# Kernel optimization log

Measured on AMD Instinct MI355X. Metric: run time of the kernel, lower is better.

Reference implementation:

```python
import jax, jax.numpy as jnp
import numpy as np

D_MODEL = 1024
NUM_HEADS = 16
HEAD_DIM = D_MODEL // NUM_HEADS
SCALE = HEAD_DIM ** -0.5
BATCH = 4096
N_MODULES = 8


def setup_inputs() -> dict:
    key = jax.random.key(0)
    ks = jax.random.split(key, 7)
    s = 1.0 / np.sqrt(D_MODEL)
    return {
        "query": jax.random.normal(ks[0], (BATCH, D_MODEL), jnp.float32),
        "kv_stack": jax.random.normal(ks[1], (N_MODULES, BATCH, D_MODEL), jnp.float32),
        "Wq": jax.random.normal(ks[2], (D_MODEL, D_MODEL), jnp.float32) * s,
        "Wk": jax.random.normal(ks[3], (D_MODEL, D_MODEL), jnp.float32) * s,
        "Wv": jax.random.normal(ks[4], (D_MODEL, D_MODEL), jnp.float32) * s,
        "Wo": jax.random.normal(ks[5], (D_MODEL, D_MODEL), jnp.float32) * s,
        "bo": jnp.zeros((D_MODEL,), jnp.float32),
    }


def reference(query, kv_stack, Wq, Wk, Wv, Wo, bo):
    # query: [B, D]; kv_stack: [M, B, D] (stacked module representations)
    B = query.shape[0]
    M = kv_stack.shape[0]
    # projections (nn.Linear: x @ W.T), split into heads; seq_len == 1
    q = (query @ Wq.T).reshape(B, NUM_HEADS, HEAD_DIM)            # [B,H,hd]
    k = jnp.einsum("mbd,ed->mbe", kv_stack, Wk).reshape(M, B, NUM_HEADS, HEAD_DIM)
    v = jnp.einsum("mbd,ed->mbe", kv_stack, Wv).reshape(M, B, NUM_HEADS, HEAD_DIM)
    # scores over the single kv position: [M,B,H,1]
    scores = jnp.einsum("bhd,mbhd->mbh", q, k)[..., None] * SCALE
    attn_weights = jax.nn.softmax(scores, axis=-1)  # softmax over size-1 axis -> ones
    attn_output = attn_weights * v                   # [M,B,H,hd] (dropout is eval/no-op)
    attn_output = attn_output.reshape(M, B, D_MODEL)
    out = jnp.einsum("mbe,oe->mbo", attn_output, Wo) + bo + query  # residual per module
    return out  # [M, B, D] (stacked in kv order instead of the dict)
```

## Files before the change

### kernel.cpp

```cpp
#include <hip/hip_runtime.h>
#include <hip/hip_bf16.h>


typedef __attribute__((ext_vector_type(4))) float f32x4;
typedef __attribute__((ext_vector_type(8))) short short8;

#define D_MODEL 1024
#define BATCH   4096
#define M_ROWS  32768

__device__ __forceinline__ short f2bf(float f) {
    union { float f; unsigned u; } x; x.f = f;
    unsigned r = (x.u + 0x7fffu + ((x.u >> 16) & 1u)) >> 16;
    return (short)r;
}

__device__ __forceinline__ unsigned bfpk(float lo, float hi) {
    __hip_bfloat162 h = __float22bfloat162_rn(make_float2(lo, hi));
    unsigned u; __builtin_memcpy(&u, &h, 4); return u;
}

__device__ __forceinline__ short8 cvt8(float4 a, float4 b) {
    union { unsigned u[4]; short8 s; } r;
    r.u[0] = bfpk(a.x, a.y);
    r.u[1] = bfpk(a.z, a.w);
    r.u[2] = bfpk(b.x, b.y);
    r.u[3] = bfpk(b.z, b.w);
    return r.s;
}

__global__ __launch_bounds__(256) void cvt_kv_kernel(
        const float* __restrict__ in, short* __restrict__ outb) {
    const long n8 = (long)M_ROWS * D_MODEL / 8;
    long i = (long)blockIdx.x * 256 + threadIdx.x;
    const long stride = (long)gridDim.x * 256;
    for (; i < n8; i += stride) {
        const float4* p = (const float4*)(in + i * 8);
        float4 a = p[0], b = p[1];
        *reinterpret_cast<short8*>(outb + i * 8) = cvt8(a, b);
    }
}

__global__ __launch_bounds__(256) void fuse_w_kernel(
        const float* __restrict__ Wo, const float* __restrict__ Wv,
        short* __restrict__ Cw) {
    __shared__ __align__(16) short Ash[64][32];
    __shared__ __align__(16) short Bsh[64][32];
    const int t = threadIdx.x;
    const int lane = t & 63;
    const int w = t >> 6;
    const int wr = w >> 1, wc = w & 1;
    const int brow = blockIdx.y * 64;
    const int bcol = blockIdx.x * 64;

    f32x4 acc[2][2];
#pragma unroll
    for (int m = 0; m < 2; ++m)
#pragma unroll
        for (int n = 0; n < 2; ++n) acc[m][n] = (f32x4)(0.0f);

    for (int kt = 0; kt < 32; ++kt) {
        const float* ga = Wo + (size_t)(brow + (t >> 2)) * D_MODEL + kt * 32 + (t & 3) * 8;
        float4 a0 = *(const float4*)ga;
        float4 a1 = *(const float4*)(ga + 4);
        float4 bv[2];
#pragma unroll
        for (int j = 0; j < 2; ++j) {
            int lin = j * 256 + t;
            int e = lin >> 4, c4 = lin & 15;
            bv[j] = *(const float4*)(Wv + (size_t)(kt * 32 + e) * D_MODEL + bcol + c4 * 4);
        }
        *reinterpret_cast<short8*>(&Ash[t >> 2][(t & 3) * 8]) = cvt8(a0, a1);
#pragma unroll
        for (int j = 0; j < 2; ++j) {
            int lin = j * 256 + t;
            int e = lin >> 4, c4 = lin & 15;
            int d = c4 * 4;
            Bsh[d + 0][e] = f2bf(bv[j].x);
            Bsh[d + 1][e] = f2bf(bv[j].y);
            Bsh[d + 2][e] = f2bf(bv[j].z);
            Bsh[d + 3][e] = f2bf(bv[j].w);
        }
        __syncthreads();
        {
            const int r = lane & 15, q = lane >> 4;
            short8 af[2], bfr[2];
#pragma unroll
            for (int m = 0; m < 2; ++m)
                af[m] = *reinterpret_cast<const short8*>(&Ash[wr * 32 + m * 16 + r][q * 8]);
#pragma unroll
            for (int n = 0; n < 2; ++n)
                bfr[n] = *reinterpret_cast<const short8*>(&Bsh[wc * 32 + n * 16 + r][q * 8]);
#pragma unroll
            for (int m = 0; m < 2; ++m)
#pragma unroll
                for (int n = 0; n < 2; ++n)
                    acc[m][n] = __builtin_amdgcn_mfma_f32_16x16x32_bf16(
                        af[m], bfr[n], acc[m][n], 0, 0, 0);
        }
        __syncthreads();
    }

    const int r = lane & 15, q = lane >> 4;
#pragma unroll
    for (int m = 0; m < 2; ++m)
#pragma unroll
        for (int n = 0; n < 2; ++n)
#pragma unroll
            for (int j = 0; j < 4; ++j) {
                int o = brow + wr * 32 + m * 16 + q * 4 + j;
                int d = bcol + wc * 32 + n * 16 + r;
                Cw[(size_t)o * D_MODEL + d] = f2bf(acc[m][n][j]);
            }
}

__global__ __launch_bounds__(256, 3) void attn_gemm_bf16(
        const short* __restrict__ kvb, const float* __restrict__ query,
        const short* __restrict__ Cw, const float* __restrict__ bo,
        float* __restrict__ out) {
    __shared__ __align__(16) short Afs[3][128][32];
    __shared__ __align__(16) short Bsh[3][128][32];
    const int t = threadIdx.x;
    const int lane = t & 63;
    const int w = t >> 6;
    const int wm = w >> 1, wn = w & 1;
    const int r = lane & 15, q = lane >> 4;

    const int L = blockIdx.x;
    const int x = L & 7, j5 = L >> 3;
    const int bx = j5 & 7;
    const int rt = (j5 >> 3) * 8 + x;
    const int brow = rt * 128;

    f32x4 acc[4][4];
#pragma unroll
    for (int m = 0; m < 4; ++m)
#pragma unroll
        for (int n = 0; n < 4; ++n) acc[m][n] = (f32x4)(0.0f);

    auto stage = [&](int kt, int buf) {
#pragma unroll
        for (int i = 0; i < 2; ++i) {
            int chunk = i * 256 + t;
            int rl = chunk >> 2, d = chunk & 3;
            int cs = d ^ ((rl >> 1) & 3);
            const short* g = kvb + (size_t)(brow + rl) * D_MODEL + kt * 32 + cs * 8;
            __builtin_amdgcn_global_load_lds(
                (const __attribute__((address_space(1))) void*)g,
                (__attribute__((address_space(3))) void*)
                    ((char*)&Afs[buf][0][0] + i * 4096 + w * 1024),
                16, 0, 0);
        }
#pragma unroll
        for (int i = 0; i < 2; ++i) {
            int chunk = i * 256 + t;
            int rl = chunk >> 2, d = chunk & 3;
            int cs = d ^ ((rl >> 1) & 3);
            const short* g = Cw + (size_t)(bx * 128 + rl) * D_MODEL + kt * 32 + cs * 8;
            __builtin_amdgcn_global_load_lds(
                (const __attribute__((address_space(1))) void*)g,
                (__attribute__((address_space(3))) void*)
                    ((char*)&Bsh[buf][0][0] + i * 4096 + w * 1024),
                16, 0, 0);
        }
    };
    auto compute = [&](int buf) {
        short8 af[4], bfr[4];
#pragma unroll
        for (int m = 0; m < 4; ++m) {
            int row = wm * 64 + m * 16 + r;
            int c = q ^ ((row >> 1) & 3);
            af[m] = *reinterpret_cast<const short8*>(&Afs[buf][row][c * 8]);
        }
#pragma unroll
        for (int n = 0; n < 4; ++n) {
            int row = wn * 64 + n * 16 + r;
            int c = q ^ ((row >> 1) & 3);
            bfr[n] = *reinterpret_cast<const short8*>(&Bsh[buf][row][c * 8]);
        }
#pragma unroll
        for (int m = 0; m < 4; ++m)
#pragma unroll
            for (int n = 0; n < 4; ++n)
                acc[m][n] = __builtin_amdgcn_mfma_f32_16x16x32_bf16(
                    af[m], bfr[n], acc[m][n], 0, 0, 0);
    };

    stage(0, 0);
    stage(1, 1);
    for (int kt = 0; kt < 32; ++kt) {
        const int bsel = kt % 3;
        if (kt < 30) {
            stage(kt + 2, (kt + 2) % 3);
            asm volatile("s_waitcnt vmcnt(8)" ::: "memory");
        } else if (kt == 30) {
            asm volatile("s_waitcnt vmcnt(4)" ::: "memory");
        } else {
            asm volatile("s_waitcnt vmcnt(0)" ::: "memory");
        }
        __builtin_amdgcn_s_barrier();
        compute(bsel);
        __builtin_amdgcn_s_barrier();
    }

#pragma unroll
    for (int n = 0; n < 4; ++n) {
        int o = bx * 128 + wn * 64 + n * 16 + r;
        float bov = bo[o];
#pragma unroll
        for (int m = 0; m < 4; ++m) {
            int gb = brow + wm * 64 + m * 16 + q * 4;
#pragma unroll
            for (int j = 0; j < 4; ++j) {
                int grow = gb + j;
                out[(size_t)grow * D_MODEL + o] =
                    acc[m][n][j] + bov +
                    query[(size_t)(grow & (BATCH - 1)) * D_MODEL + o];
            }
        }
    }
}

__global__ __launch_bounds__(256, 4) void attn_gemm_f32(
        const float* __restrict__ kv, const float* __restrict__ query,
        const short* __restrict__ Cw, const float* __restrict__ bo,
        float* __restrict__ out) {
    __shared__ __align__(16) float Afs[64][64];
    __shared__ __align__(16) short Bsh[128][64];
    const int t = threadIdx.x;
    const int lane = t & 63;
    const int w = t >> 6;
    const int wr = w >> 1, wc = w & 1;
    const int r = lane & 15, q = lane >> 4;

    const int L = blockIdx.x;
    const int x = L & 7, j5 = L >> 3;
    const int bx = j5 & 7;
    const int rt = (j5 >> 3) * 8 + x;
    const int brow = rt * 64;

    f32x4 acc[2][4];
#pragma unroll
    for (int m = 0; m < 2; ++m)
#pragma unroll
        for (int n = 0; n < 4; ++n) acc[m][n] = (f32x4)(0.0f);

    for (int kt = 0; kt < 16; ++kt) {
#pragma unroll
        for (int i = 0; i < 4; ++i) {
            int chunk = i * 256 + t;
            int rl = chunk >> 4, d = chunk & 15;
            int cs = d ^ (rl & 7);
            const float* g = kv + (size_t)(brow + rl) * D_MODEL + kt * 64 + cs * 4;
            __builtin_amdgcn_global_load_lds(
                (const __attribute__((address_space(1))) void*)g,
                (__attribute__((address_space(3))) void*)
                    ((char*)&Afs[0][0] + i * 4096 + w * 1024),
                16, 0, 0);
        }
#pragma unroll
        for (int i = 0; i < 4; ++i) {
            int chunk = i * 256 + t;
            int rl = chunk >> 3, d = chunk & 7;
            int cs = d ^ (rl & 7);
            const short* g = Cw + (size_t)(bx * 128 + rl) * D_MODEL + kt * 64 + cs * 8;
            __builtin_amdgcn_global_load_lds(
                (const __attribute__((address_space(1))) void*)g,
                (__attribute__((address_space(3))) void*)
                    ((char*)&Bsh[0][0] + i * 4096 + w * 1024),
                16, 0, 0);
        }
        __syncthreads();
#pragma unroll
        for (int s = 0; s < 2; ++s) {
            short8 af[2], bfr[4];
#pragma unroll
            for (int m = 0; m < 2; ++m) {
                int row = wr * 32 + m * 16 + r;
                int c0 = (s * 8 + q * 2) ^ (row & 7);
                int c1 = (s * 8 + q * 2 + 1) ^ (row & 7);
                float4 lo = *(const float4*)&Afs[row][c0 * 4];
                float4 hi = *(const float4*)&Afs[row][c1 * 4];
                af[m] = cvt8(lo, hi);
            }
#pragma unroll
            for (int n = 0; n < 4; ++n) {
                int row = wc * 64 + n * 16 + r;
                int c = (s * 4 + q) ^ (row & 7);
                bfr[n] = *reinterpret_cast<const short8*>(&Bsh[row][c * 8]);
            }
#pragma unroll
            for (int m = 0; m < 2; ++m)
#pragma unroll
                for (int n = 0; n < 4; ++n)
                    acc[m][n] = __builtin_amdgcn_mfma_f32_16x16x32_bf16(
                        af[m], bfr[n], acc[m][n], 0, 0, 0);
        }
        __syncthreads();
    }

#pragma unroll
    for (int n = 0; n < 4; ++n) {
        int o = bx * 128 + wc * 64 + n * 16 + r;
        float bov = bo[o];
#pragma unroll
        for (int m = 0; m < 2; ++m) {
            int gb = brow + wr * 32 + m * 16 + q * 4;
#pragma unroll
            for (int j = 0; j < 4; ++j) {
                int grow = gb + j;
                out[(size_t)grow * D_MODEL + o] =
                    acc[m][n][j] + bov +
                    query[(size_t)(grow & (BATCH - 1)) * D_MODEL + o];
            }
        }
    }
}

extern "C" void kernel_launch(void* const* d_in, const int* in_sizes, int n_in,
                              void* d_out, int out_size, void* d_ws, size_t ws_size,
                              hipStream_t stream) {
    int kv_i = 1, q_i = 0, bo_i = 6;
    int w_i[4] = {2, 3, 4, 5};
    int nw = 0;
    for (int i = 0; i < n_in; ++i) {
        long s = in_sizes[i];
        if (s == 33554432) kv_i = i;
        else if (s == 4194304) q_i = i;
        else if (s == 1024) bo_i = i;
        else if (s == 1048576 && nw < 4) w_i[nw++] = i;
    }
    const float* query = (const float*)d_in[q_i];
    const float* kv    = (const float*)d_in[kv_i];
    const float* Wv    = (const float*)d_in[w_i[2]];
    const float* Wo    = (const float*)d_in[w_i[3]];
    const float* bo    = (const float*)d_in[bo_i];
    short* Cw  = (short*)d_ws;
    float* out = (float*)d_out;

    fuse_w_kernel<<<dim3(16, 16), dim3(256), 0, stream>>>(Wo, Wv, Cw);

    const size_t need = (size_t)2 * 1024 * 1024 + (size_t)M_ROWS * D_MODEL * 2;
    if (ws_size >= need) {
        short* kvb = (short*)((char*)d_ws + 2 * 1024 * 1024);
        cvt_kv_kernel<<<dim3(2048), dim3(256), 0, stream>>>(kv, kvb);
        attn_gemm_bf16<<<dim3(2048), dim3(256), 0, stream>>>(kvb, query, Cw, bo, out);
    } else {
        attn_gemm_f32<<<dim3(4096), dim3(256), 0, stream>>>(kv, query, Cw, bo, out);
    }
}
```

Before: 178.8 us.

## Merge weight fusion and kv conversion into one launch; use double buffering in GEMM

Merges the Wo·Wv fusion GEMM and the fp32→bf16 kv conversion into a single pre-kernel, with extra blocks doing the conversion, so the two run concurrently and one launch is saved. The main bf16 GEMM drops from a triple-buffered to a double-buffered LDS pipeline and raises the occupancy hint from 3 to 4 blocks per CU. The smaller LDS footprint is meant to allow more resident blocks. The cost is a shallower prefetch distance, which can expose more global-load latency.

```diff
diff --git a/kernel.cpp b/kernel.cpp
--- a/kernel.cpp
+++ b/kernel.cpp
@@ -29,29 +29,29 @@
     return r.s;
 }
 
-__global__ __launch_bounds__(256) void cvt_kv_kernel(
-        const float* __restrict__ in, short* __restrict__ outb) {
-    const long n8 = (long)M_ROWS * D_MODEL / 8;
-    long i = (long)blockIdx.x * 256 + threadIdx.x;
-    const long stride = (long)gridDim.x * 256;
-    for (; i < n8; i += stride) {
-        const float4* p = (const float4*)(in + i * 8);
-        float4 a = p[0], b = p[1];
-        *reinterpret_cast<short8*>(outb + i * 8) = cvt8(a, b);
-    }
-}
-
-__global__ __launch_bounds__(256) void fuse_w_kernel(
+__global__ __launch_bounds__(256) void pre_kernel(
         const float* __restrict__ Wo, const float* __restrict__ Wv,
-        short* __restrict__ Cw) {
+        short* __restrict__ Cw,
+        const float* __restrict__ kv, short* __restrict__ kvb) {
+    const int t = threadIdx.x;
+    if (blockIdx.x >= 256) {
+        const long n8 = (long)M_ROWS * D_MODEL / 8;
+        long i = (long)(blockIdx.x - 256) * 256 + t;
+        const long stride = 2048L * 256;
+        for (; i < n8; i += stride) {
+            const float4* p = (const float4*)(kv + i * 8);
+            float4 a = p[0], b = p[1];
+            *reinterpret_cast<short8*>(kvb + i * 8) = cvt8(a, b);
+        }
+        return;
+    }
     __shared__ __align__(16) short Ash[64][32];
     __shared__ __align__(16) short Bsh[64][32];
-    const int t = threadIdx.x;
     const int lane = t & 63;
     const int w = t >> 6;
     const int wr = w >> 1, wc = w & 1;
-    const int brow = blockIdx.y * 64;
-    const int bcol = blockIdx.x * 64;
+    const int brow = (blockIdx.x >> 4) * 64;
+    const int bcol = (blockIdx.x & 15) * 64;
 
     f32x4 acc[2][2];
 #pragma unroll
@@ -114,12 +114,12 @@
             }
 }
 
-__global__ __launch_bounds__(256, 3) void attn_gemm_bf16(
+__global__ __launch_bounds__(256, 4) void attn_gemm_bf16(
         const short* __restrict__ kvb, const float* __restrict__ query,
         const short* __restrict__ Cw, const float* __restrict__ bo,
         float* __restrict__ out) {
-    __shared__ __align__(16) short Afs[3][128][32];
-    __shared__ __align__(16) short Bsh[3][128][32];
+    __shared__ __align__(16) short Afs[2][128][32];
+    __shared__ __align__(16) short Bsh[2][128][32];
     const int t = threadIdx.x;
     const int lane = t & 63;
     const int w = t >> 6;
@@ -187,19 +187,16 @@
     };
 
     stage(0, 0);
-    stage(1, 1);
     for (int kt = 0; kt < 32; ++kt) {
-        const int bsel = kt % 3;
-        if (kt < 30) {
-            stage(kt + 2, (kt + 2) % 3);
-            asm volatile("s_waitcnt vmcnt(8)" ::: "memory");
-        } else if (kt == 30) {
+        const int cur = kt & 1;
+        if (kt < 31) {
+            stage(kt + 1, cur ^ 1);
             asm volatile("s_waitcnt vmcnt(4)" ::: "memory");
         } else {
             asm volatile("s_waitcnt vmcnt(0)" ::: "memory");
         }
         __builtin_amdgcn_s_barrier();
-        compute(bsel);
+        compute(cur);
         __builtin_amdgcn_s_barrier();
     }
 
@@ -338,14 +335,13 @@
     short* Cw  = (short*)d_ws;
     float* out = (float*)d_out;
 
-    fuse_w_kernel<<<dim3(16, 16), dim3(256), 0, stream>>>(Wo, Wv, Cw);
-
     const size_t need = (size_t)2 * 1024 * 1024 + (size_t)M_ROWS * D_MODEL * 2;
     if (ws_size >= need) {
         short* kvb = (short*)((char*)d_ws + 2 * 1024 * 1024);
-        cvt_kv_kernel<<<dim3(2048), dim3(256), 0, stream>>>(kv, kvb);
+        pre_kernel<<<dim3(2304), dim3(256), 0, stream>>>(Wo, Wv, Cw, kv, kvb);
         attn_gemm_bf16<<<dim3(2048), dim3(256), 0, stream>>>(kvb, query, Cw, bo, out);
     } else {
+        pre_kernel<<<dim3(256), dim3(256), 0, stream>>>(Wo, Wv, Cw, kv, nullptr);
         attn_gemm_f32<<<dim3(4096), dim3(256), 0, stream>>>(kv, query, Cw, bo, out);
     }
 }
```

Measured after the change: 180.0 us. Within noise of the previous version (+0.7%).
